# Optimization experiments

Measured on AMD Instinct MI355X. Metric: run time of the kernel, lower is better.

Reference implementation:

```python
import jax, jax.numpy as jnp
import numpy as np

N_NODE = 50000
N_EDGE = 1000000
IN_CH = 64
HID_CH = 64
NUM_REL = 8


def setup_inputs() -> dict:
    key = jax.random.key(0)
    k1, k2, k3, k4 = jax.random.split(key, 4)
    x = jax.random.normal(k1, (N_NODE, IN_CH), dtype=jnp.float32)
    W = jax.random.normal(k2, (NUM_REL, IN_CH, HID_CH), dtype=jnp.float32)
    edge_index = jax.random.randint(k3, (2, N_EDGE), 0, N_NODE, dtype=jnp.int64)
    rel = jax.random.randint(k4, (N_EDGE,), 0, NUM_REL, dtype=jnp.int64)
    return {"x": x, "W": W, "edge_index": edge_index, "rel": rel,
            "num_node": N_NODE, "num_edge": N_EDGE}


def reference(x, W, edge_index, rel, num_node, num_edge):
    # Original: per-edge gather of x[src] and W[rel], per-edge vec-mat multiply,
    # then scatter-add into dst. Equivalent math, but we avoid materializing the
    # huge per-edge [E, in, hid] weight tensor: transform all nodes under every
    # relation first ([R, N, hid] is small), then gather the right (rel, src) row.
    src = edge_index[0, :num_edge]
    dst = edge_index[1, :num_edge]
    r = rel[:num_edge]
    # [R, N, hid] = all-node features transformed by each relation's weight
    xw = jnp.einsum('ni,rih->rnh', x, W)
    # per-edge transformed feature: [E, hid]
    transformed = xw[r, src]
    # scatter-add over destination nodes -> [num_node, hid]
    out = jax.ops.segment_sum(transformed, dst, num_segments=num_node)
    return out
```

## Files before the change

kernel.cpp:

```cpp
#include <hip/hip_runtime.h>
#include <hip/hip_bf16.h>

#define NREL 8
#define CH   64
#define NPB  16

typedef unsigned int uint32;
typedef __attribute__((ext_vector_type(8))) short bf16x8;
typedef __attribute__((ext_vector_type(4))) float f32x4;
union U4 { uint4 u; bf16x8 v; };

static __device__ __forceinline__ uint32 packbf(float a, float b) {
    uint32 ua = __float_as_uint(a), ub = __float_as_uint(b);
    ua = (ua + 0x7fffu + ((ua >> 16) & 1u)) >> 16;
    ub = (ub + 0x7fffu + ((ub >> 16) & 1u)) & 0xffff0000u;
    return ua | ub;
}
static __device__ __forceinline__ float bflo(uint32 w) { return __uint_as_float(w << 16); }
static __device__ __forceinline__ float bfhi(uint32 w) { return __uint_as_float(w & 0xffff0000u); }

__global__ __launch_bounds__(256) void prep2_k(
    const float* __restrict__ x, uint32* __restrict__ xbf,
    const float* __restrict__ Wf, uint32* __restrict__ Bfrag,
    const int* __restrict__ ei, int* __restrict__ ccnt,
    int n2, int nE, int nXB)
{
    const int b = blockIdx.x;
    if (b < 16) {
        const int idx  = b * 256 + threadIdx.x;
        const int lane = idx & 63;
        const int c    = (idx >> 6) & 3;
        const int ks   = idx >> 8;
        const int col  = c * 16 + (lane & 15);
        const int k0   = ks * 32 + (lane >> 4) * 8;
        uint4 o;
        o.x = packbf(Wf[(k0 + 0) * 64 + col], Wf[(k0 + 1) * 64 + col]);
        o.y = packbf(Wf[(k0 + 2) * 64 + col], Wf[(k0 + 3) * 64 + col]);
        o.z = packbf(Wf[(k0 + 4) * 64 + col], Wf[(k0 + 5) * 64 + col]);
        o.w = packbf(Wf[(k0 + 6) * 64 + col], Wf[(k0 + 7) * 64 + col]);
        *(uint4*)(Bfrag + (size_t)idx * 4) = o;
    } else if (b < 16 + nXB) {
        const int i = (b - 16) * 256 + threadIdx.x;
        if (i < n2) {
            const float2 v = ((const float2*)x)[i];
            xbf[i] = packbf(v.x, v.y);
        }
    } else {
        __shared__ int h[256];
        h[threadIdx.x] = 0;
        __syncthreads();
        const int cb = b - 16 - nXB;
        for (int e = cb * 256 + threadIdx.x; e < nE; e += 256 * 256)
            atomicAdd(&h[ei[nE + e] >> 8], 1);
        __syncthreads();
        const int c = threadIdx.x;
        if (h[c]) atomicAdd(&ccnt[c], h[c]);
    }
}

__global__ __launch_bounds__(256) void bin_k(
    const int* __restrict__ ei, const int* __restrict__ rel,
    const int* __restrict__ ccnt, int* __restrict__ cur0,
    uint32* __restrict__ binned, int nE)
{
    __shared__ uint32        ent[4096];
    __shared__ unsigned char cid[4096];
    __shared__ int lh[256], lb[256], lc[256], cbl[256], wsum[4];

    const int t = threadIdx.x;

    {
        const int v = ccnt[t];
        int s = v;
        #pragma unroll
        for (int off = 1; off < 64; off <<= 1) {
            const int u = __shfl_up(s, off, 64);
            if ((t & 63) >= off) s += u;
        }
        if ((t & 63) == 63) wsum[t >> 6] = s;
        lh[t] = 0;
        __syncthreads();
        int addv = 0;
        #pragma unroll
        for (int w = 0; w < 3; ++w)
            if (w < (t >> 6)) addv += wsum[w];
        cbl[t] = s - v + addv;
    }
    __syncthreads();

    const int base = blockIdx.x * 4096;
    #pragma unroll
    for (int i = 0; i < 16; ++i) {
        const int idx = t + i * 256;
        const int e   = base + idx;
        if (e < nE) {
            const int dst = ei[nE + e];
            ent[idx] = ((uint32)(dst & 255) << 24) | ((uint32)rel[e] << 16) | (uint32)ei[e];
            const int c = dst >> 8;
            cid[idx] = (unsigned char)c;
            atomicAdd(&lh[c], 1);
        } else {
            cid[idx] = 255;
        }
    }
    __syncthreads();

    if (lh[t]) lb[t] = cbl[t] + atomicAdd(&cur0[t], lh[t]);
    lc[t] = 0;
    __syncthreads();

    #pragma unroll
    for (int i = 0; i < 16; ++i) {
        const int idx = t + i * 256;
        const int c   = cid[idx];
        if (c != 255) {
            const int off = atomicAdd(&lc[c], 1);
            binned[lb[c] + off] = ent[idx];
        }
    }
}

__global__ __launch_bounds__(1024) void fsort_k(
    const uint32* __restrict__ binned, const int* __restrict__ ccnt,
    int* __restrict__ start, int* __restrict__ sorted, int NC, int nE)
{
    __shared__ int fh[2048], fex[2048], fcur[2048], ws[16], red[16], nsh[2];
    const int c = blockIdx.x;
    const int t = threadIdx.x;

    {
        int v = (t < c) ? ccnt[t] : 0;
        #pragma unroll
        for (int off = 32; off > 0; off >>= 1) v += __shfl_down(v, off, 64);
        if ((t & 63) == 0) red[t >> 6] = v;
        fh[t] = 0; fh[t + 1024] = 0;
        __syncthreads();
        if (t == 0) {
            int s = 0;
            #pragma unroll
            for (int i = 0; i < 16; ++i) s += red[i];
            nsh[0] = s;
            nsh[1] = s + ccnt[c];
        }
    }
    __syncthreads();
    const int n0 = nsh[0];
    const int n1 = nsh[1];

    for (int j = n0 + t; j < n1; j += 1024) {
        const uint32 en = binned[j];
        atomicAdd(&fh[((en >> 24) << 3) | ((en >> 16) & 7)], 1);
    }
    __syncthreads();

    const int a = fh[2 * t], b = fh[2 * t + 1];
    const int p = a + b;
    int s = p;
    #pragma unroll
    for (int off = 1; off < 64; off <<= 1) {
        const int u = __shfl_up(s, off, 64);
        if ((t & 63) >= off) s += u;
    }
    if ((t & 63) == 63) ws[t >> 6] = s;
    __syncthreads();
    if (t < 16) {
        const int vv = ws[t];
        int ss = vv;
        #pragma unroll
        for (int off = 1; off < 16; off <<= 1) {
            const int u = __shfl_up(ss, off, 16);
            if (t >= off) ss += u;
        }
        ws[t] = ss - vv;
    }
    __syncthreads();
    const int ep = s - p + ws[t >> 6];
    fex[2 * t] = ep; fex[2 * t + 1] = ep + a;
    __syncthreads();

    fcur[t] = fex[t]; fcur[t + 1024] = fex[t + 1024];
    {
        const int k0 = c << 11;
        start[k0 + t]        = n0 + fex[t];
        start[k0 + t + 1024] = n0 + fex[t + 1024];
    }
    if (c == NC - 1 && t == 0) start[NC << 11] = n1;
    __syncthreads();

    for (int j = n0 + t; j < n1; j += 1024) {
        const uint32 en = binned[j];
        const int fk  = ((en >> 24) << 3) | ((en >> 16) & 7);
        const int off = atomicAdd(&fcur[fk], 1);
        sorted[n0 + off] = (int)(en & 0x7FFFFu);
    }
}

#define AGG_FLUSH()                                                          \
    {                                                                        \
        const int widx = (row * 256 + (prev * 2 + (l32 >> 4)) * 16 +         \
                          (l32 & 15)) ^ ((row & 7) << 2);                    \
        als[widx] = packbf(a0, a1);                                          \
    }

#define AGG_PROCESS(eu, uu)                                                  \
    {                                                                        \
        const int r_ = (int)((eu) >> 16);                                    \
        if (r_ != prev) {                                                    \
            if (prev >= 0) AGG_FLUSH();                                      \
            a0 = 0.f; a1 = 0.f;                                              \
            prev = r_;                                                       \
        }                                                                    \
        a0 += bflo(uu); a1 += bfhi(uu);                                      \
    }

__global__ __launch_bounds__(512) void aggemm_k(
    const uint32* __restrict__ xbf, const int* __restrict__ start,
    const int* __restrict__ sorted, const uint32* __restrict__ Bfrag,
    float* __restrict__ out, int nN)
{
    __shared__ uint32 als[NPB * 256];

    const int t      = threadIdx.x;
    const int row    = t >> 5;
    const int l32    = t & 31;
    const int n_base = blockIdx.x * NPB;
    const int n      = n_base + row;

    #pragma unroll
    for (int z = 0; z < 8; ++z)
        als[(row * 256 + z * 32 + l32) ^ ((row & 7) << 2)] = 0u;

    if (n < nN) {
        const int kb = n * NREL;
        const int b0 = start[kb];
        const int b8 = start[kb + 8];

        int   prev = -1;
        float a0 = 0.f, a1 = 0.f;

        for (int base = b0; base < b8; base += 32) {
            const int cnt = min(32, b8 - base);
            const int jj  = base + l32;
            const uint32 ev = (jj < b8) ? (uint32)sorted[jj] : 0u;

            int j = 0;
            for (; j + 8 <= cnt; j += 8) {
                const uint32 e0 = __shfl(ev, j + 0, 32);
                const uint32 e1 = __shfl(ev, j + 1, 32);
                const uint32 e2 = __shfl(ev, j + 2, 32);
                const uint32 e3 = __shfl(ev, j + 3, 32);
                const uint32 e4 = __shfl(ev, j + 4, 32);
                const uint32 e5 = __shfl(ev, j + 5, 32);
                const uint32 e6 = __shfl(ev, j + 6, 32);
                const uint32 e7 = __shfl(ev, j + 7, 32);
                const uint32 u0 = xbf[(size_t)(e0 & 0xFFFFu) * 32 + l32];
                const uint32 u1 = xbf[(size_t)(e1 & 0xFFFFu) * 32 + l32];
                const uint32 u2 = xbf[(size_t)(e2 & 0xFFFFu) * 32 + l32];
                const uint32 u3 = xbf[(size_t)(e3 & 0xFFFFu) * 32 + l32];
                const uint32 u4 = xbf[(size_t)(e4 & 0xFFFFu) * 32 + l32];
                const uint32 u5 = xbf[(size_t)(e5 & 0xFFFFu) * 32 + l32];
                const uint32 u6 = xbf[(size_t)(e6 & 0xFFFFu) * 32 + l32];
                const uint32 u7 = xbf[(size_t)(e7 & 0xFFFFu) * 32 + l32];
                AGG_PROCESS(e0, u0);
                AGG_PROCESS(e1, u1);
                AGG_PROCESS(e2, u2);
                AGG_PROCESS(e3, u3);
                AGG_PROCESS(e4, u4);
                AGG_PROCESS(e5, u5);
                AGG_PROCESS(e6, u6);
                AGG_PROCESS(e7, u7);
            }
            for (; j + 4 <= cnt; j += 4) {
                const uint32 e0 = __shfl(ev, j + 0, 32);
                const uint32 e1 = __shfl(ev, j + 1, 32);
                const uint32 e2 = __shfl(ev, j + 2, 32);
                const uint32 e3 = __shfl(ev, j + 3, 32);
                const uint32 u0 = xbf[(size_t)(e0 & 0xFFFFu) * 32 + l32];
                const uint32 u1 = xbf[(size_t)(e1 & 0xFFFFu) * 32 + l32];
                const uint32 u2 = xbf[(size_t)(e2 & 0xFFFFu) * 32 + l32];
                const uint32 u3 = xbf[(size_t)(e3 & 0xFFFFu) * 32 + l32];
                AGG_PROCESS(e0, u0);
                AGG_PROCESS(e1, u1);
                AGG_PROCESS(e2, u2);
                AGG_PROCESS(e3, u3);
            }
            for (; j < cnt; ++j) {
                const uint32 e = __shfl(ev, j, 32);
                const uint32 u = xbf[(size_t)(e & 0xFFFFu) * 32 + l32];
                AGG_PROCESS(e, u);
            }
        }
        if (prev >= 0) AGG_FLUSH();
    }
    __syncthreads();

    if (t < 256) {
        const int lane = t & 63;
        const int w    = t >> 6;
        const int rl   = lane & 15;
        const int kq   = lane >> 4;

        f32x4 acc = (f32x4){0.f, 0.f, 0.f, 0.f};
        const uint32* bp = Bfrag + (size_t)lane * 4;

        #pragma unroll
        for (int ks = 0; ks < 16; ++ks) {
            const int aidx = (rl * 256 + ks * 16 + kq * 4) ^ ((rl & 7) << 2);
            U4 ua, ub;
            ua.u = *(const uint4*)(als + aidx);
            ub.u = *(const uint4*)(bp + (size_t)(ks * 4 + w) * 256);
            acc = __builtin_amdgcn_mfma_f32_16x16x32_bf16(ua.v, ub.v, acc, 0, 0, 0);
        }

        #pragma unroll
        for (int reg = 0; reg < 4; ++reg) {
            const int rr = kq * 4 + reg;
            const int nn = n_base + rr;
            if (nn < nN)
                out[(size_t)nn * 64 + w * 16 + rl] = acc[reg];
        }
    }
}

__global__ __launch_bounds__(256) void rgcn_direct_kernel(
    const float* __restrict__ x, const float* __restrict__ W,
    const int* __restrict__ ei, const int* __restrict__ rel,
    float* __restrict__ out, int nE, int nWaves)
{
    const int w    = (int)((blockIdx.x * 256u + threadIdx.x) >> 6);
    const int lane = threadIdx.x & 63;

    for (int e = w; e < nE; e += nWaves) {
        const int src = ei[e];
        const int dst = ei[nE + e];
        const int r   = rel[e];
        const float* xrow = x + (size_t)src * CH;
        const float* wcol = W + ((size_t)r << 12) + lane;
        float acc = 0.f;
        #pragma unroll
        for (int i = 0; i < CH; ++i) acc += xrow[i] * wcol[i * CH];
        atomicAdd(out + (size_t)dst * CH + lane, acc);
    }
}

static inline size_t align256(size_t v) { return (v + 255) & ~(size_t)255; }

extern "C" void kernel_launch(void* const* d_in, const int* in_sizes, int n_in,
                              void* d_out, int out_size, void* d_ws, size_t ws_size,
                              hipStream_t stream) {
    const float* x   = (const float*)d_in[0];
    const float* W   = (const float*)d_in[1];
    const int*   ei  = (const int*)d_in[2];
    const int*   rel = (const int*)d_in[3];
    float*       out = (float*)d_out;

    const int nN = in_sizes[0] / CH;
    const int nE = in_sizes[3];
    const int NC = (nN + 255) >> 8;

    const size_t sz_xbf    = align256((size_t)nN * 32 * sizeof(uint32));
    const size_t sz_start  = align256(((size_t)NC * 2048 + 2) * sizeof(int));
    const size_t sz_binned = align256((size_t)nE * sizeof(uint32));
    const size_t sz_sorted = align256((size_t)nE * sizeof(int));
    const size_t sz_bfrag  = align256((size_t)16384 * sizeof(uint32));
    const size_t sz_ccnt   = align256(256 * sizeof(int));
    const size_t sz_cur0   = align256(256 * sizeof(int));
    const size_t need = sz_xbf + sz_start + sz_binned + sz_sorted +
                        sz_bfrag + sz_ccnt + sz_cur0;

    if (ws_size >= need && nN <= 65024 && NC <= 254) {
        char* p = (char*)d_ws;
        uint32* xbf    = (uint32*)p;  p += sz_xbf;
        int*    start  = (int*)p;     p += sz_start;
        uint32* binned = (uint32*)p;  p += sz_binned;
        int*    sorted = (int*)p;     p += sz_sorted;
        uint32* Bfrag  = (uint32*)p;  p += sz_bfrag;
        int*    ccnt   = (int*)p;     p += sz_ccnt;
        int*    cur0   = (int*)p;

        hipMemsetAsync(ccnt, 0, sz_ccnt + sz_cur0, stream);

        const int n2  = nN * 32;
        const int nXB = (n2 + 255) / 256;
        prep2_k<<<16 + nXB + 256, 256, 0, stream>>>(
            x, xbf, W, Bfrag, ei, ccnt, n2, nE, nXB);

        bin_k<<<(nE + 4095) / 4096, 256, 0, stream>>>(ei, rel, ccnt, cur0, binned, nE);
        fsort_k<<<NC, 1024, 0, stream>>>(binned, ccnt, start, sorted, NC, nE);

        aggemm_k<<<(nN + NPB - 1) / NPB, 512, 0, stream>>>(
            xbf, start, sorted, Bfrag, out, nN);
    } else {
        hipMemsetAsync(out, 0, (size_t)out_size * sizeof(float), stream);
        const int blocks = 2048;
        const int nWaves = blocks * (256 / 64);
        rgcn_direct_kernel<<<blocks, 256, 0, stream>>>(x, W, ei, rel, out, nE, nWaves);
    }
}
```

Before: 79.97 us.

## Split each node's edge aggregation across two wave halves with xor-shuffle reduction

The aggregation kernel now gives each destination node a full 64-lane wavefront instead of 32 lanes. Each half of the wave gathers alternate edges, and partial sums are combined with a cross-half shuffle whenever a relation segment ends. This doubles the gather parallelism per node and halves the serial edge loop length, aiming to hide gather latency better. In exchange the block size grows to 1024 threads, and there is extra shuffle and branch overhead at relation boundaries.

```diff
diff --git a/kernel.cpp b/kernel.cpp
--- a/kernel.cpp
+++ b/kernel.cpp
@@ -195,25 +195,38 @@
     }
 }
 
-#define AGG_FLUSH()                                                          \
+#define PAIR_FLUSH(rr)                                                       \
     {                                                                        \
-        const int widx = (row * 256 + (prev * 2 + (l32 >> 4)) * 16 +         \
-                          (l32 & 15)) ^ ((row & 7) << 2);                    \
-        als[widx] = packbf(a0, a1);                                          \
-    }
-
-#define AGG_PROCESS(eu, uu)                                                  \
+        const float c0 = a0 + __shfl_xor(a0, 32, 64);                        \
+        const float c1 = a1 + __shfl_xor(a1, 32, 64);                        \
+        if (!half) {                                                         \
+            const int widx = (row * 256 + ((rr) * 2 + (l32 >> 4)) * 16 +     \
+                              (l32 & 15)) ^ ((row & 7) << 2);                \
+            als[widx] = packbf(c0, c1);                                      \
+        }                                                                    \
+    }
+
+#define PAIR_STEP(elo, ehi, uu)                                              \
     {                                                                        \
-        const int r_ = (int)((eu) >> 16);                                    \
-        if (r_ != prev) {                                                    \
-            if (prev >= 0) AGG_FLUSH();                                      \
+        const int rlo = (int)((elo) >> 16);                                  \
+        const int rhi = (int)((ehi) >> 16);                                  \
+        if (rlo != prev) {                                                   \
+            if (prev >= 0) PAIR_FLUSH(prev);                                 \
             a0 = 0.f; a1 = 0.f;                                              \
-            prev = r_;                                                       \
+            prev = rlo;                                                      \
         }                                                                    \
-        a0 += bflo(uu); a1 += bfhi(uu);                                      \
-    }
-
-__global__ __launch_bounds__(512) void aggemm_k(
+        if (rhi == rlo) {                                                    \
+            a0 += bflo(uu); a1 += bfhi(uu);                                  \
+        } else {                                                             \
+            if (!half) { a0 += bflo(uu); a1 += bfhi(uu); }                   \
+            PAIR_FLUSH(rlo);                                                 \
+            a0 = 0.f; a1 = 0.f;                                              \
+            prev = rhi;                                                      \
+            if (half) { a0 += bflo(uu); a1 += bfhi(uu); }                    \
+        }                                                                    \
+    }
+
+__global__ __launch_bounds__(1024) void aggemm_k(
     const uint32* __restrict__ xbf, const int* __restrict__ start,
     const int* __restrict__ sorted, const uint32* __restrict__ Bfrag,
     float* __restrict__ out, int nN)
@@ -221,14 +234,16 @@
     __shared__ uint32 als[NPB * 256];
 
     const int t      = threadIdx.x;
-    const int row    = t >> 5;
+    const int row    = t >> 6;
+    const int lane   = t & 63;
     const int l32    = t & 31;
+    const int half   = (t >> 5) & 1;
     const int n_base = blockIdx.x * NPB;
     const int n      = n_base + row;
 
     #pragma unroll
-    for (int z = 0; z < 8; ++z)
-        als[(row * 256 + z * 32 + l32) ^ ((row & 7) << 2)] = 0u;
+    for (int z = 0; z < 4; ++z)
+        als[(row * 256 + z * 64 + lane) ^ ((row & 7) << 2)] = 0u;
 
     if (n < nN) {
         const int kb = n * NREL;
@@ -238,70 +253,55 @@
         int   prev = -1;
         float a0 = 0.f, a1 = 0.f;
 
-        for (int base = b0; base < b8; base += 32) {
-            const int cnt = min(32, b8 - base);
-            const int jj  = base + l32;
+        for (int base = b0; base < b8; base += 64) {
+            const int cnt = min(64, b8 - base);
+            const int jj  = base + lane;
             const uint32 ev = (jj < b8) ? (uint32)sorted[jj] : 0u;
 
             int j = 0;
             for (; j + 8 <= cnt; j += 8) {
-                const uint32 e0 = __shfl(ev, j + 0, 32);
-                const uint32 e1 = __shfl(ev, j + 1, 32);
-                const uint32 e2 = __shfl(ev, j + 2, 32);
-                const uint32 e3 = __shfl(ev, j + 3, 32);
-                const uint32 e4 = __shfl(ev, j + 4, 32);
-                const uint32 e5 = __shfl(ev, j + 5, 32);
-                const uint32 e6 = __shfl(ev, j + 6, 32);
-                const uint32 e7 = __shfl(ev, j + 7, 32);
-                const uint32 u0 = xbf[(size_t)(e0 & 0xFFFFu) * 32 + l32];
-                const uint32 u1 = xbf[(size_t)(e1 & 0xFFFFu) * 32 + l32];
-                const uint32 u2 = xbf[(size_t)(e2 & 0xFFFFu) * 32 + l32];
-                const uint32 u3 = xbf[(size_t)(e3 & 0xFFFFu) * 32 + l32];
-                const uint32 u4 = xbf[(size_t)(e4 & 0xFFFFu) * 32 + l32];
-                const uint32 u5 = xbf[(size_t)(e5 & 0xFFFFu) * 32 + l32];
-                const uint32 u6 = xbf[(size_t)(e6 & 0xFFFFu) * 32 + l32];
-                const uint32 u7 = xbf[(size_t)(e7 & 0xFFFFu) * 32 + l32];
-                AGG_PROCESS(e0, u0);
-                AGG_PROCESS(e1, u1);
-                AGG_PROCESS(e2, u2);
-                AGG_PROCESS(e3, u3);
-                AGG_PROCESS(e4, u4);
-                AGG_PROCESS(e5, u5);
-                AGG_PROCESS(e6, u6);
-                AGG_PROCESS(e7, u7);
+                const uint32 eA = __shfl(ev, j + 0, 64), eB = __shfl(ev, j + 1, 64);
+                const uint32 eC = __shfl(ev, j + 2, 64), eD = __shfl(ev, j + 3, 64);
+                const uint32 eE = __shfl(ev, j + 4, 64), eF = __shfl(ev, j + 5, 64);
+                const uint32 eG = __shfl(ev, j + 6, 64), eH = __shfl(ev, j + 7, 64);
+                const uint32 u0 = xbf[(size_t)((half ? eB : eA) & 0xFFFFu) * 32 + l32];
+                const uint32 u1 = xbf[(size_t)((half ? eD : eC) & 0xFFFFu) * 32 + l32];
+                const uint32 u2 = xbf[(size_t)((half ? eF : eE) & 0xFFFFu) * 32 + l32];
+                const uint32 u3 = xbf[(size_t)((half ? eH : eG) & 0xFFFFu) * 32 + l32];
+                PAIR_STEP(eA, eB, u0);
+                PAIR_STEP(eC, eD, u1);
+                PAIR_STEP(eE, eF, u2);
+                PAIR_STEP(eG, eH, u3);
             }
-            for (; j + 4 <= cnt; j += 4) {
-                const uint32 e0 = __shfl(ev, j + 0, 32);
-                const uint32 e1 = __shfl(ev, j + 1, 32);
-                const uint32 e2 = __shfl(ev, j + 2, 32);
-                const uint32 e3 = __shfl(ev, j + 3, 32);
-                const uint32 u0 = xbf[(size_t)(e0 & 0xFFFFu) * 32 + l32];
-                const uint32 u1 = xbf[(size_t)(e1 & 0xFFFFu) * 32 + l32];
-                const uint32 u2 = xbf[(size_t)(e2 & 0xFFFFu) * 32 + l32];
-                const uint32 u3 = xbf[(size_t)(e3 & 0xFFFFu) * 32 + l32];
-                AGG_PROCESS(e0, u0);
-                AGG_PROCESS(e1, u1);
-                AGG_PROCESS(e2, u2);
-                AGG_PROCESS(e3, u3);
+            for (; j + 2 <= cnt; j += 2) {
+                const uint32 eA = __shfl(ev, j, 64), eB = __shfl(ev, j + 1, 64);
+                const uint32 u0 = xbf[(size_t)((half ? eB : eA) & 0xFFFFu) * 32 + l32];
+                PAIR_STEP(eA, eB, u0);
             }
-            for (; j < cnt; ++j) {
-                const uint32 e = __shfl(ev, j, 32);
+            if (j < cnt) {
+                const uint32 e = __shfl(ev, j, 64);
                 const uint32 u = xbf[(size_t)(e & 0xFFFFu) * 32 + l32];
-                AGG_PROCESS(e, u);
+                const int r_ = (int)(e >> 16);
+                if (r_ != prev) {
+                    if (prev >= 0) PAIR_FLUSH(prev);
+                    a0 = 0.f; a1 = 0.f;
+                    prev = r_;
+                }
+                if (!half) { a0 += bflo(u); a1 += bfhi(u); }
             }
         }
-        if (prev >= 0) AGG_FLUSH();
+        if (prev >= 0) PAIR_FLUSH(prev);
     }
     __syncthreads();
 
     if (t < 256) {
-        const int lane = t & 63;
-        const int w    = t >> 6;
-        const int rl   = lane & 15;
-        const int kq   = lane >> 4;
+        const int ln = t & 63;
+        const int w  = t >> 6;
+        const int rl = ln & 15;
+        const int kq = ln >> 4;
 
         f32x4 acc = (f32x4){0.f, 0.f, 0.f, 0.f};
-        const uint32* bp = Bfrag + (size_t)lane * 4;
+        const uint32* bp = Bfrag + (size_t)ln * 4;
 
         #pragma unroll
         for (int ks = 0; ks < 16; ++ks) {
@@ -388,7 +388,7 @@
         bin_k<<<(nE + 4095) / 4096, 256, 0, stream>>>(ei, rel, ccnt, cur0, binned, nE);
         fsort_k<<<NC, 1024, 0, stream>>>(binned, ccnt, start, sorted, NC, nE);
 
-        aggemm_k<<<(nN + NPB - 1) / NPB, 512, 0, stream>>>(
+        aggemm_k<<<(nN + NPB - 1) / NPB, 1024, 0, stream>>>(
             xbf, start, sorted, Bfrag, out, nN);
     } else {
         hipMemsetAsync(out, 0, (size_t)out_size * sizeof(float), stream);
```

Result: slower. 93.57 us (+17.0%).
